# Optimization experiments

Hardware: AMD Instinct MI355X
Metric: run time of the kernel (lower is better)

Reference implementation:

```python
import jax, jax.numpy as jnp
import numpy as np
import math

N, E, IN, OUT, T, R = 50000, 500000, 128, 128, 8, 8
SQRT_DK = math.sqrt(OUT)


def setup_inputs() -> dict:
    key = jax.random.key(0)
    ks = jax.random.split(key, 12)
    return {
        "h": jax.random.normal(ks[0], (N, IN), jnp.float32),
        "adj": jax.random.randint(ks[1], (2, E), 0, N),
        "edge_type": jax.random.randint(ks[2], (E,), 0, R),
        "node_type": jax.random.randint(ks[3], (N,), 0, T),
        "src_type": jax.random.randint(ks[4], (E,), 0, T),
        "dst_type": jax.random.randint(ks[5], (E,), 0, T),
        # params (torch.rand -> uniform[0,1), torch.ones -> ones)
        "k_weights": jax.random.uniform(ks[6], (T, IN, OUT), jnp.float32),
        "q_weights": jax.random.uniform(ks[7], (T, IN, OUT), jnp.float32),
        "v_weights": jax.random.uniform(ks[8], (T, IN, OUT), jnp.float32),
        "a_weights": jax.random.uniform(ks[9], (T, OUT, OUT), jnp.float32),
        "relation_pri": jnp.ones((R, 1), jnp.float32),
        "relation_att": jax.random.uniform(ks[10], (R, OUT, OUT), jnp.float32),
        "relation_msg": jax.random.uniform(ks[11], (R, OUT, OUT), jnp.float32),
        "skip": jnp.ones((T,), jnp.float32),
    }


def _per_type(x, W, types):
    # x: [N,d], W: [T,d,f], types: [N] -> [N,f]
    # project by every type then select; avoids materializing a [N,d,f] gather
    all_proj = jnp.einsum('nd,tdf->tnf', x, W)  # [T,N,f]
    return all_proj[types, jnp.arange(x.shape[0])]


def _segment_softmax(scores, seg, num_segments):
    m = jax.ops.segment_max(scores, seg, num_segments=num_segments)
    m = jnp.where(jnp.isfinite(m), m, 0.0)  # empty segments
    ex = jnp.exp(scores - m[seg])
    denom = jax.ops.segment_sum(ex, seg, num_segments=num_segments)
    return ex / denom[seg]


def reference(h, adj, edge_type, node_type, src_type, dst_type,
              k_weights, q_weights, v_weights, a_weights,
              relation_pri, relation_att, relation_msg, skip):
    n = h.shape[0]
    src, dst = adj[0], adj[1]
    # per-node-type K/Q/V projections
    k = _per_type(h, k_weights, node_type)  # [N,OUT]
    q = _per_type(h, q_weights, node_type)
    v = _per_type(h, v_weights, node_type)
    # per-relation projections computed on nodes, then gathered per edge
    # (equivalent to k_j @ relation_att[edge_type] without an [E,D,D] gather)
    kA = jnp.einsum('nd,rdf->rnf', k, relation_att)[edge_type, src]  # [E,OUT]
    vM = jnp.einsum('nd,rdf->rnf', v, relation_msg)[edge_type, src]  # [E,OUT]
    q_i = q[dst]                                                     # [E,OUT]
    score = jnp.sum(kA * q_i, axis=-1) * relation_pri[edge_type, 0] / SQRT_DK  # [E]
    seg = dst * R + edge_type  # segment softmax keyed by (dst node, rel type)
    alpha = _segment_softmax(score, seg, n * R)  # [E]
    agg = jax.ops.segment_sum(vM * alpha[:, None], dst, num_segments=n)  # [N,OUT]
    # update: per-node-type output transform with sigmoid(skip) gate
    trans = _per_type(agg, a_weights, node_type)
    return trans * jax.nn.sigmoid(skip[node_type])[:, None]
```

## Files before the change

kernel.cpp:

```cpp
#include <hip/hip_runtime.h>
#include <math.h>


#define N_NODES 50000
#define N_EDGES 500000
#define DIM 128
#define TT 8
#define RR 8
#define RSQRT_DK 0.08838834764831845f

#define CHUNK_GRID 399
#define NODE_LIST_LEN (CHUNK_GRID * 128)
#define GRID_E ((N_EDGES + 255) / 256)
#define SCAN_BLOCKS ((N_NODES + 255) / 256)

#define NR3_CHUNKS 112
#define NR3_ROWS 448
#define NR3_ITERS 7

#define OFF_KA 0
#define OFF_HF 0
#define OFF_VM 25600000
#define OFF_KF 25600000
#define OFF_QF 51200000
#define OFF_AGGF 54400000
#define OFF_VF 54400000
#define OFF_ATTT 57600000
#define OFF_MSGT 57700000
#define OFF_WVT 57800000
#define OFF_WAT 57900000
#define OFF_INT 58000000
#define IO_NLIST 0
#define IO_CNT_N 51072
#define IO_CUR_N 51080
#define IO_POFF_N 51088
#define IO_DCNT 51104
#define IO_DCUR 101104
#define IO_DOFF 151104
#define IO_DPR 201104
#define IO_BLKSUM 701104
#define IO_BLKOFF 701360

typedef _Float16 half8 __attribute__((ext_vector_type(8)));
typedef _Float16 half4 __attribute__((ext_vector_type(4)));
typedef float f32x4 __attribute__((ext_vector_type(4)));

__global__ void init_kernel(int* wsi) {
    int i = blockIdx.x * blockDim.x + threadIdx.x;
    if (i < NODE_LIST_LEN) wsi[IO_NLIST + i] = -1;
    if (i < 32) wsi[IO_CNT_N + i] = 0;
    if (i < 100000) wsi[IO_DCNT + i] = 0;
}

__global__ void convert_kernel(const float* __restrict__ att,
                               const float* __restrict__ msg,
                               const float* __restrict__ Wv,
                               const float* __restrict__ Wa,
                               _Float16* __restrict__ attT,
                               _Float16* __restrict__ msgT,
                               _Float16* __restrict__ WvT,
                               _Float16* __restrict__ WaT) {
    int i = blockIdx.x * 256 + threadIdx.x;
    if (i >= RR * DIM * DIM) return;
    int td = i >> 14, d = (i >> 7) & 127, f = i & 127;
    int tr = (td << 14) + (f << 7) + d;
    attT[tr] = (_Float16)att[i];
    msgT[tr] = (_Float16)msg[i];
    WvT[tr] = (_Float16)Wv[i];
    WaT[tr] = (_Float16)Wa[i];
}

__global__ void hconv_kernel(const float* __restrict__ h,
                             _Float16* __restrict__ hF) {
    int i = blockIdx.x * 256 + threadIdx.x;
    if (i < N_NODES * DIM / 4) {
        float4 v = ((const float4*)h)[i];
        half4 o;
        o[0] = (_Float16)v.x; o[1] = (_Float16)v.y;
        o[2] = (_Float16)v.z; o[3] = (_Float16)v.w;
        *(half4*)(hF + (size_t)i * 4) = o;
    }
}

__global__ void hist_kernel(const int* __restrict__ ntype,
                            const int* __restrict__ adj, int* wsi) {
    __shared__ int cn[TT];
    int tid = threadIdx.x;
    if (tid < TT) cn[tid] = 0;
    __syncthreads();
    int i = blockIdx.x * blockDim.x + tid;
    if (i < N_NODES) atomicAdd(&cn[ntype[i]], 1);
    if (i < N_EDGES) atomicAdd(&wsi[IO_DCNT + adj[N_EDGES + i]], 1);
    __syncthreads();
    if (tid < TT && cn[tid] > 0) atomicAdd(&wsi[IO_CNT_N + tid], cn[tid]);
}

__global__ void offsets_kernel(int* wsi) {
    int off = 0;
    for (int t = 0; t < TT; ++t) {
        wsi[IO_POFF_N + t] = off;
        off += ((wsi[IO_CNT_N + t] + 127) >> 7) << 7;
    }
}

__global__ __launch_bounds__(256) void scanA_kernel(int* wsi) {
    __shared__ int tmp[256];
    int tid = threadIdx.x;
    int i = blockIdx.x * 256 + tid;
    int v = (i < N_NODES) ? wsi[IO_DCNT + i] : 0;
    tmp[tid] = v;
    __syncthreads();
    for (int off = 1; off < 256; off <<= 1) {
        int t = (tid >= off) ? tmp[tid - off] : 0;
        __syncthreads();
        tmp[tid] += t;
        __syncthreads();
    }
    if (i < N_NODES) wsi[IO_DOFF + i] = tmp[tid] - v;
    if (tid == 255) wsi[IO_BLKSUM + blockIdx.x] = tmp[255];
}

__global__ __launch_bounds__(256) void scanB_kernel(int* wsi) {
    __shared__ int tmp[256];
    int tid = threadIdx.x;
    int v = (tid < SCAN_BLOCKS) ? wsi[IO_BLKSUM + tid] : 0;
    tmp[tid] = v;
    __syncthreads();
    for (int off = 1; off < 256; off <<= 1) {
        int t = (tid >= off) ? tmp[tid - off] : 0;
        __syncthreads();
        tmp[tid] += t;
        __syncthreads();
    }
    wsi[IO_BLKOFF + tid] = tmp[tid] - v;
}

__global__ __launch_bounds__(256) void scanC_kernel(int* wsi) {
    int i = blockIdx.x * 256 + threadIdx.x;
    if (i < N_NODES) wsi[IO_DOFF + i] += wsi[IO_BLKOFF + blockIdx.x];
}

__global__ void scatter_kernel(const int* __restrict__ ntype,
                               const int* __restrict__ etype,
                               const int* __restrict__ adj, int* wsi) {
    __shared__ int cn[TT], bn[TT];
    int tid = threadIdx.x;
    if (tid < TT) cn[tid] = 0;
    __syncthreads();
    int i = blockIdx.x * blockDim.x + tid;
    int t = -1, rnk = 0;
    if (i < N_NODES) {
        t = ntype[i];
        rnk = atomicAdd(&cn[t], 1);
    }
    __syncthreads();
    if (tid < TT && cn[tid] > 0) bn[tid] = atomicAdd(&wsi[IO_CUR_N + tid], cn[tid]);
    __syncthreads();
    if (t >= 0)
        wsi[IO_NLIST + wsi[IO_POFF_N + t] + bn[t] + rnk] = i;
    if (i < N_EDGES) {
        int d = adj[N_EDGES + i];
        int pos = wsi[IO_DOFF + d] + atomicAdd(&wsi[IO_DCUR + d], 1);
        wsi[IO_DPR + pos] = (adj[i] << 3) | etype[i];
    }
}

__global__ __launch_bounds__(256, 4) void kq_f32_kernel(
    const float* __restrict__ h, const int* __restrict__ ntype,
    const float* __restrict__ Wk, const float* __restrict__ Wq,
    const int* __restrict__ nlist, _Float16* __restrict__ kout,
    _Float16* __restrict__ qout) {
    __shared__ float hl[64][DIM + 4];
    __shared__ int nid[64];
    int tid = threadIdx.x;
    int base = blockIdx.x * 64;
    if (tid < 64) nid[tid] = nlist[base + tid];
    __syncthreads();
    if (nid[0] < 0) return;
    int t = ntype[nid[0]];

    for (int r2 = 0; r2 < 64; r2 += 2) {
        int row = r2 + (tid >> 7);
        int col = tid & 127;
        int n = nid[row];
        if (n < 0) n = 0;
        hl[row][col] = h[(size_t)n * DIM + col];
    }
    __syncthreads();
    int te = tid >> 5, tc = tid & 31;

    int w = blockIdx.y;
    const float* W = (w == 0 ? Wk : Wq) + (size_t)t * DIM * DIM;
    const float4* W4 = (const float4*)W;
    _Float16* O = (w == 0 ? kout : qout);
    float acc[8][4] = {};
    float4 cur0 = W4[0 * 32 + tc];
    float4 cur1 = W4[1 * 32 + tc];
    float4 cur2 = W4[2 * 32 + tc];
    float4 cur3 = W4[3 * 32 + tc];
    for (int i = 0; i < DIM; i += 4) {
        int ip = (i + 4 < DIM) ? (i + 4) : 0;
        float4 nxt0 = W4[(ip + 0) * 32 + tc];
        float4 nxt1 = W4[(ip + 1) * 32 + tc];
        float4 nxt2 = W4[(ip + 2) * 32 + tc];
        float4 nxt3 = W4[(ip + 3) * 32 + tc];
#pragma unroll
        for (int j = 0; j < 8; ++j) {
            float4 hv = *(const float4*)&hl[te * 8 + j][i];
            acc[j][0] += hv.x * cur0.x;
            acc[j][1] += hv.x * cur0.y;
            acc[j][2] += hv.x * cur0.z;
            acc[j][3] += hv.x * cur0.w;
            acc[j][0] += hv.y * cur1.x;
            acc[j][1] += hv.y * cur1.y;
            acc[j][2] += hv.y * cur1.z;
            acc[j][3] += hv.y * cur1.w;
            acc[j][0] += hv.z * cur2.x;
            acc[j][1] += hv.z * cur2.y;
            acc[j][2] += hv.z * cur2.z;
            acc[j][3] += hv.z * cur2.w;
            acc[j][0] += hv.w * cur3.x;
            acc[j][1] += hv.w * cur3.y;
            acc[j][2] += hv.w * cur3.z;
            acc[j][3] += hv.w * cur3.w;
        }
        cur0 = nxt0;
        cur1 = nxt1;
        cur2 = nxt2;
        cur3 = nxt3;
    }
#pragma unroll
    for (int j = 0; j < 8; ++j) {
        int n = nid[te * 8 + j];
        if (n >= 0) {
            half4 o;
            o[0] = (_Float16)acc[j][0];
            o[1] = (_Float16)acc[j][1];
            o[2] = (_Float16)acc[j][2];
            o[3] = (_Float16)acc[j][3];
            *(half4*)(O + (size_t)n * DIM + tc * 4) = o;
        }
    }
}

__global__ __launch_bounds__(256) void vproj_kernel(
    const _Float16* __restrict__ hF, const int* __restrict__ ntype,
    const _Float16* __restrict__ WvT, const int* __restrict__ nlist,
    _Float16* __restrict__ vout) {
    __shared__ int nid[128];
    int tid = threadIdx.x;
    if (tid < 128) nid[tid] = nlist[blockIdx.x * 128 + tid];
    __syncthreads();
    if (nid[0] < 0) return;
    int t = ntype[nid[0]];
    int wv = tid >> 6, lane = tid & 63, l16 = lane & 15, quad = lane >> 4;
    int r0 = wv * 32;
    int nA[2];
#pragma unroll
    for (int m = 0; m < 2; ++m) nA[m] = nid[r0 + m * 16 + l16];
    const _Float16* B = WvT + (t << 14);
    f32x4 acc[2][8];
#pragma unroll
    for (int m = 0; m < 2; ++m)
#pragma unroll
        for (int c = 0; c < 8; ++c) acc[m][c] = (f32x4){0.f, 0.f, 0.f, 0.f};
    for (int kk = 0; kk < 4; ++kk) {
        int kb = kk * 32 + quad * 8;
        half8 a[2];
#pragma unroll
        for (int m = 0; m < 2; ++m)
            a[m] = (nA[m] >= 0)
                       ? *(const half8*)(hF + (size_t)nA[m] * DIM + kb)
                       : (half8){0, 0, 0, 0, 0, 0, 0, 0};
#pragma unroll
        for (int c = 0; c < 8; ++c) {
            half8 b = *(const half8*)(B + (c * 16 + l16) * DIM + kb);
#pragma unroll
            for (int m = 0; m < 2; ++m)
                acc[m][c] = __builtin_amdgcn_mfma_f32_16x16x32_f16(
                    a[m], b, acc[m][c], 0, 0, 0);
        }
    }
#pragma unroll
    for (int m = 0; m < 2; ++m)
#pragma unroll
        for (int c = 0; c < 8; ++c)
#pragma unroll
            for (int rg = 0; rg < 4; ++rg) {
                int node = nid[r0 + m * 16 + quad * 4 + rg];
                if (node >= 0)
                    vout[(size_t)node * DIM + c * 16 + l16] =
                        (_Float16)acc[m][c][rg];
            }
}

__global__ __launch_bounds__(256, 2) void nr_gemm3_kernel(
    const _Float16* __restrict__ A, const _Float16* __restrict__ B8,
    _Float16* __restrict__ Out, const float* __restrict__ pri, int isU) {
    __shared__ _Float16 stage[4][16][136];
    int bid = blockIdx.x;
    int rel = bid / NR3_CHUNKS;
    int chunk = bid - rel * NR3_CHUNKS;
    float scale = isU ? pri[rel] * RSQRT_DK : 1.0f;
    const _Float16* Bb = B8 + (rel << 14);
    int tid = threadIdx.x;
    int wv = tid >> 6, lane = tid & 63;
    int l16 = lane & 15, quad = lane >> 4;

    half8 bfrag[8][4];
#pragma unroll
    for (int c = 0; c < 8; ++c)
#pragma unroll
        for (int kk = 0; kk < 4; ++kk)
            bfrag[c][kk] =
                *(const half8*)(Bb + (c * 16 + l16) * DIM + kk * 32 + quad * 8);

    _Float16* Orel = Out + (size_t)rel * N_NODES * DIM;
    int base = chunk * NR3_ROWS + wv * 16;

    half8 aNow[4], aNext[4];
    {
        int nodeA = base + l16;
#pragma unroll
        for (int kk = 0; kk < 4; ++kk)
            aNow[kk] = (nodeA < N_NODES)
                           ? *(const half8*)(A + (size_t)nodeA * DIM +
                                             kk * 32 + quad * 8)
                           : (half8){0, 0, 0, 0, 0, 0, 0, 0};
    }

    for (int it = 0; it < NR3_ITERS; ++it) {
        int row0 = base + it * 64;
        if (it + 1 < NR3_ITERS) {
            int nodeA = row0 + 64 + l16;
#pragma unroll
            for (int kk = 0; kk < 4; ++kk)
                aNext[kk] = (nodeA < N_NODES)
                                ? *(const half8*)(A + (size_t)nodeA * DIM +
                                                  kk * 32 + quad * 8)
                                : (half8){0, 0, 0, 0, 0, 0, 0, 0};
        }
        f32x4 acc[8];
#pragma unroll
        for (int c = 0; c < 8; ++c) acc[c] = (f32x4){0.f, 0.f, 0.f, 0.f};
#pragma unroll
        for (int kk = 0; kk < 4; ++kk)
#pragma unroll
            for (int c = 0; c < 8; ++c)
                acc[c] = __builtin_amdgcn_mfma_f32_16x16x32_f16(
                    bfrag[c][kk], aNow[kk], acc[c], 0, 0, 0);
#pragma unroll
        for (int c = 0; c < 8; ++c) {
            half4 o;
#pragma unroll
            for (int rg = 0; rg < 4; ++rg)
                o[rg] = (_Float16)(acc[c][rg] * scale);
            *(half4*)&stage[wv][l16][c * 16 + quad * 4] = o;
        }
        _Float16* Op = Orel + (size_t)row0 * DIM;
#pragma unroll
        for (int s = 0; s < 4; ++s) {
            int row = s * 4 + quad;
            if (row0 + row < N_NODES) {
                half8 v = *(const half8*)&stage[wv][row][l16 * 8];
                *(half8*)(Op + (size_t)row * DIM + l16 * 8) = v;
            }
        }
#pragma unroll
        for (int kk = 0; kk < 4; ++kk) aNow[kk] = aNext[kk];
    }
}

__global__ __launch_bounds__(256) void attend_kernel(
    const _Float16* __restrict__ KA, const _Float16* __restrict__ qF,
    const _Float16* __restrict__ VMF, const int* __restrict__ dpr,
    const int* __restrict__ doff, const int* __restrict__ dcnt,
    _Float16* __restrict__ aggF) {
    int wv = threadIdx.x >> 6, lane = threadIdx.x & 63;
    int dst = blockIdx.x * 4 + wv;
    if (dst >= N_NODES) return;
    int l16 = lane & 15, g = lane >> 4, l8 = lane & 7;
    int beg = doff[dst], cnt = dcnt[dst];

    half8 qv = *(const half8*)(qF + (size_t)dst * DIM + l16 * 8);

    float m_own = -3e38f, sum_own = 0.f;
    float s0 = 0.f, s1 = 0.f, s2 = 0.f;
    int p0 = 0, p1 = 0, p2 = 0;

    for (int j0 = 0; j0 < cnt; j0 += 4) {
        int j = j0 + g;
        bool valid = j < cnt;
        int pr = valid ? dpr[beg + j] : 0;
        int src = pr >> 3, rel = pr & 7;
        half8 kv = *(const half8*)(KA + ((size_t)rel * N_NODES + src) * DIM +
                                   l16 * 8);
        float sa = 0.f, sb = 0.f;
#pragma unroll
        for (int i = 0; i < 4; ++i) sa += (float)kv[i] * (float)qv[i];
#pragma unroll
        for (int i = 4; i < 8; ++i) sb += (float)kv[i] * (float)qv[i];
        float s = sa + sb;
        s += __shfl_xor(s, 1, 16);
        s += __shfl_xor(s, 2, 16);
        s += __shfl_xor(s, 4, 16);
        s += __shfl_xor(s, 8, 16);
        if (!valid) s = -3e38f;
        int slot = j0 >> 6;
        int idx = (j0 >> 2) & 15;
        if (l16 == idx) {
            if (slot == 0) { s0 = s; p0 = pr; }
            else if (slot == 1) { s1 = s; p1 = pr; }
            else if (slot == 2) { s2 = s; p2 = pr; }
        }
        if (valid && l8 == rel) {
            if (s > m_own) {
                sum_own *= __expf(m_own - s);
                m_own = s;
            }
            sum_own += __expf(s - m_own);
        }
    }
    {
        float m2 = __shfl_xor(m_own, 16, 64);
        float t2 = __shfl_xor(sum_own, 16, 64);
        float mn = fmaxf(m_own, m2);
        sum_own = sum_own * __expf(m_own - mn) + t2 * __expf(m2 - mn);
        m_own = mn;
        m2 = __shfl_xor(m_own, 32, 64);
        t2 = __shfl_xor(sum_own, 32, 64);
        mn = fmaxf(m_own, m2);
        sum_own = sum_own * __expf(m_own - mn) + t2 * __expf(m2 - mn);
        m_own = mn;
    }
    float inv_own = (sum_own > 0.f) ? 1.f / sum_own : 0.f;

    float acc[8] = {0.f, 0.f, 0.f, 0.f, 0.f, 0.f, 0.f, 0.f};
    for (int j0 = 0; j0 < cnt; j0 += 4) {
        int j = j0 + g;
        bool valid = j < cnt;
        int slot = j0 >> 6;
        int idx = (j0 >> 2) & 15;
        float s;
        int pr;
        if (slot < 3) {
            float sv = (slot == 0) ? s0 : (slot == 1) ? s1 : s2;
            int pv = (slot == 0) ? p0 : (slot == 1) ? p1 : p2;
            s = __shfl(sv, idx, 16);
            pr = __shfl(pv, idx, 16);
        } else {
            pr = valid ? dpr[beg + j] : 0;
            int src = pr >> 3, rel = pr & 7;
            half8 kv = *(const half8*)(KA +
                                       ((size_t)rel * N_NODES + src) * DIM +
                                       l16 * 8);
            float sa = 0.f, sb = 0.f;
#pragma unroll
            for (int i = 0; i < 4; ++i) sa += (float)kv[i] * (float)qv[i];
#pragma unroll
            for (int i = 4; i < 8; ++i) sb += (float)kv[i] * (float)qv[i];
            s = sa + sb;
            s += __shfl_xor(s, 1, 16);
            s += __shfl_xor(s, 2, 16);
            s += __shfl_xor(s, 4, 16);
            s += __shfl_xor(s, 8, 16);
        }
        int rel = pr & 7, src = pr >> 3;
        float mr = __shfl(m_own, rel, 8);
        float iv = __shfl(inv_own, rel, 8);
        float alpha = valid ? __expf(s - mr) * iv : 0.f;
        half8 v = *(const half8*)(VMF + ((size_t)rel * N_NODES + src) * DIM +
                                  l16 * 8);
#pragma unroll
        for (int i = 0; i < 8; ++i) acc[i] += alpha * (float)v[i];
    }
#pragma unroll
    for (int i = 0; i < 8; ++i) {
        acc[i] += __shfl_xor(acc[i], 16, 64);
        acc[i] += __shfl_xor(acc[i], 32, 64);
    }
    if (g == 0) {
        half8 o;
#pragma unroll
        for (int i = 0; i < 8; ++i) o[i] = (_Float16)acc[i];
        *(half8*)(aggF + (size_t)dst * DIM + l16 * 8) = o;
    }
}

__global__ __launch_bounds__(256) void out_kernel(
    const _Float16* __restrict__ aggF, const int* __restrict__ ntype,
    const _Float16* __restrict__ WaT, const float* __restrict__ skip,
    const int* __restrict__ nlist, float* __restrict__ out) {
    __shared__ int nid[128];
    int tid = threadIdx.x;
    if (tid < 128) nid[tid] = nlist[blockIdx.x * 128 + tid];
    __syncthreads();
    if (nid[0] < 0) return;
    int t = ntype[nid[0]];
    float sig = 1.f / (1.f + __expf(-skip[t]));
    int wv = tid >> 6, lane = tid & 63, l16 = lane & 15, quad = lane >> 4;
    int r0 = wv * 32;
    int nA[2];
#pragma unroll
    for (int m = 0; m < 2; ++m) nA[m] = nid[r0 + m * 16 + l16];
    const _Float16* B = WaT + (t << 14);
    f32x4 acc[2][8];
#pragma unroll
    for (int m = 0; m < 2; ++m)
#pragma unroll
        for (int c = 0; c < 8; ++c) acc[m][c] = (f32x4){0.f, 0.f, 0.f, 0.f};
    for (int kk = 0; kk < 4; ++kk) {
        int kb = kk * 32 + quad * 8;
        half8 a[2];
#pragma unroll
        for (int m = 0; m < 2; ++m)
            a[m] = (nA[m] >= 0)
                       ? *(const half8*)(aggF + (size_t)nA[m] * DIM + kb)
                       : (half8){0, 0, 0, 0, 0, 0, 0, 0};
#pragma unroll
        for (int c = 0; c < 8; ++c) {
            half8 b = *(const half8*)(B + (c * 16 + l16) * DIM + kb);
#pragma unroll
            for (int m = 0; m < 2; ++m)
                acc[m][c] = __builtin_amdgcn_mfma_f32_16x16x32_f16(
                    a[m], b, acc[m][c], 0, 0, 0);
        }
    }
#pragma unroll
    for (int m = 0; m < 2; ++m)
#pragma unroll
        for (int c = 0; c < 8; ++c)
#pragma unroll
            for (int rg = 0; rg < 4; ++rg) {
                int node = nid[r0 + m * 16 + quad * 4 + rg];
                if (node >= 0)
                    out[(size_t)node * DIM + c * 16 + l16] =
                        acc[m][c][rg] * sig;
            }
}

extern "C" void kernel_launch(void* const* d_in, const int* in_sizes, int n_in,
                              void* d_out, int out_size, void* d_ws,
                              size_t ws_size, hipStream_t stream) {
    const float* h = (const float*)d_in[0];
    const int* adj = (const int*)d_in[1];
    const int* etype = (const int*)d_in[2];
    const int* ntype = (const int*)d_in[3];
    const float* Wk = (const float*)d_in[6];
    const float* Wq = (const float*)d_in[7];
    const float* Wv = (const float*)d_in[8];
    const float* Wa = (const float*)d_in[9];
    const float* pri = (const float*)d_in[10];
    const float* att = (const float*)d_in[11];
    const float* msg = (const float*)d_in[12];
    const float* skip = (const float*)d_in[13];
    float* out = (float*)d_out;

    int* wsi = (int*)d_ws + OFF_INT;
    _Float16* wsh = (_Float16*)d_ws;
    _Float16* KA = wsh + (size_t)OFF_KA * 2;
    _Float16* hF = wsh + (size_t)OFF_HF * 2;
    _Float16* VMF = wsh + (size_t)OFF_VM * 2;
    _Float16* kF = wsh + (size_t)OFF_KF * 2;
    _Float16* qF = wsh + (size_t)OFF_QF * 2;
    _Float16* aggF = wsh + (size_t)OFF_AGGF * 2;
    _Float16* vF = wsh + (size_t)OFF_VF * 2;
    _Float16* attT = wsh + (size_t)OFF_ATTT * 2;
    _Float16* msgT = wsh + (size_t)OFF_MSGT * 2;
    _Float16* WvT = wsh + (size_t)OFF_WVT * 2;
    _Float16* WaT = wsh + (size_t)OFF_WAT * 2;

    init_kernel<<<(100000 + 255) / 256, 256, 0, stream>>>(wsi);
    convert_kernel<<<(RR * DIM * DIM + 255) / 256, 256, 0, stream>>>(
        att, msg, Wv, Wa, attT, msgT, WvT, WaT);
    hconv_kernel<<<(N_NODES * DIM / 4 + 255) / 256, 256, 0, stream>>>(h, hF);
    hist_kernel<<<GRID_E, 256, 0, stream>>>(ntype, adj, wsi);
    offsets_kernel<<<1, 1, 0, stream>>>(wsi);
    scanA_kernel<<<SCAN_BLOCKS, 256, 0, stream>>>(wsi);
    scanB_kernel<<<1, 256, 0, stream>>>(wsi);
    scanC_kernel<<<SCAN_BLOCKS, 256, 0, stream>>>(wsi);
    scatter_kernel<<<GRID_E, 256, 0, stream>>>(ntype, etype, adj, wsi);
    {
        dim3 g(CHUNK_GRID * 2, 2);
        kq_f32_kernel<<<g, 256, 0, stream>>>(h, ntype, Wk, Wq,
                                             wsi + IO_NLIST, kF, qF);
    }
    vproj_kernel<<<CHUNK_GRID, 256, 0, stream>>>(hF, ntype, WvT,
                                                 wsi + IO_NLIST, vF);
    nr_gemm3_kernel<<<RR * NR3_CHUNKS, 256, 0, stream>>>(kF, attT, KA, pri, 1);
    nr_gemm3_kernel<<<RR * NR3_CHUNKS, 256, 0, stream>>>(vF, msgT, VMF, pri, 0);
    attend_kernel<<<(N_NODES + 3) / 4, 256, 0, stream>>>(
        KA, qF, VMF, wsi + IO_DPR, wsi + IO_DOFF, wsi + IO_DCNT, aggF);
    out_kernel<<<CHUNK_GRID, 256, 0, stream>>>(aggF, ntype, WaT, skip,
                                               wsi + IO_NLIST, out);
}
```

Measured before the change: 375.6 us.

## Compute K/Q projections with split-fp16 MFMA instead of FP32 FMA loops

Replaces the scalar FP32 K/Q projection kernel with an MFMA kernel that splits inputs and weights into fp16 hi/lo parts and sums three products (hi*hi, hi*lo, lo*hi) to keep near-FP32 accuracy. New conversion work writes the hLo residual for h and hi/lo transposed copies of Wk/Wq into the workspace. This trades extra memory traffic for the residual tensor, plus one extra launch, against moving the dominant FLOPs onto matrix cores. The output stores are scalar fp16 writes scattered per node row, which may be less efficient than the old vector stores.

```diff
diff --git a/kernel.cpp b/kernel.cpp
--- a/kernel.cpp
+++ b/kernel.cpp
@@ -22,6 +22,11 @@
 #define OFF_HF 0
 #define OFF_VM 25600000
 #define OFF_KF 25600000
+#define OFF_HLO 28800000
+#define OFF_WKHI 48000000
+#define OFF_WKLO 48100000
+#define OFF_WQHI 48200000
+#define OFF_WQLO 48300000
 #define OFF_QF 51200000
 #define OFF_AGGF 54400000
 #define OFF_VF 54400000
@@ -70,15 +75,41 @@
     WaT[tr] = (_Float16)Wa[i];
 }
 
+__global__ void convert2_kernel(const float* __restrict__ Wk,
+                                const float* __restrict__ Wq,
+                                _Float16* __restrict__ WkHiT,
+                                _Float16* __restrict__ WkLoT,
+                                _Float16* __restrict__ WqHiT,
+                                _Float16* __restrict__ WqLoT) {
+    int i = blockIdx.x * 256 + threadIdx.x;
+    if (i >= TT * DIM * DIM) return;
+    int td = i >> 14, d = (i >> 7) & 127, f = i & 127;
+    int tr = (td << 14) + (f << 7) + d;
+    float xk = Wk[i];
+    _Float16 hk = (_Float16)xk;
+    WkHiT[tr] = hk;
+    WkLoT[tr] = (_Float16)(xk - (float)hk);
+    float xq = Wq[i];
+    _Float16 hq = (_Float16)xq;
+    WqHiT[tr] = hq;
+    WqLoT[tr] = (_Float16)(xq - (float)hq);
+}
+
 __global__ void hconv_kernel(const float* __restrict__ h,
-                             _Float16* __restrict__ hF) {
+                             _Float16* __restrict__ hF,
+                             _Float16* __restrict__ hLo) {
     int i = blockIdx.x * 256 + threadIdx.x;
     if (i < N_NODES * DIM / 4) {
         float4 v = ((const float4*)h)[i];
-        half4 o;
+        half4 o, r;
         o[0] = (_Float16)v.x; o[1] = (_Float16)v.y;
         o[2] = (_Float16)v.z; o[3] = (_Float16)v.w;
+        r[0] = (_Float16)(v.x - (float)o[0]);
+        r[1] = (_Float16)(v.y - (float)o[1]);
+        r[2] = (_Float16)(v.z - (float)o[2]);
+        r[3] = (_Float16)(v.w - (float)o[3]);
         *(half4*)(hF + (size_t)i * 4) = o;
+        *(half4*)(hLo + (size_t)i * 4) = r;
     }
 }
 
@@ -165,82 +196,71 @@
     }
 }
 
-__global__ __launch_bounds__(256, 4) void kq_f32_kernel(
-    const float* __restrict__ h, const int* __restrict__ ntype,
-    const float* __restrict__ Wk, const float* __restrict__ Wq,
+__global__ __launch_bounds__(256) void kq_mfma_kernel(
+    const _Float16* __restrict__ hHi, const _Float16* __restrict__ hLo,
+    const int* __restrict__ ntype,
+    const _Float16* __restrict__ WkHiT, const _Float16* __restrict__ WkLoT,
+    const _Float16* __restrict__ WqHiT, const _Float16* __restrict__ WqLoT,
     const int* __restrict__ nlist, _Float16* __restrict__ kout,
     _Float16* __restrict__ qout) {
-    __shared__ float hl[64][DIM + 4];
-    __shared__ int nid[64];
-    int tid = threadIdx.x;
-    int base = blockIdx.x * 64;
-    if (tid < 64) nid[tid] = nlist[base + tid];
+    __shared__ int nid[128];
+    int tid = threadIdx.x;
+    if (tid < 128) nid[tid] = nlist[blockIdx.x * 128 + tid];
     __syncthreads();
     if (nid[0] < 0) return;
     int t = ntype[nid[0]];
-
-    for (int r2 = 0; r2 < 64; r2 += 2) {
-        int row = r2 + (tid >> 7);
-        int col = tid & 127;
-        int n = nid[row];
-        if (n < 0) n = 0;
-        hl[row][col] = h[(size_t)n * DIM + col];
-    }
-    __syncthreads();
-    int te = tid >> 5, tc = tid & 31;
-
+    int wv = tid >> 6, lane = tid & 63, l16 = lane & 15, quad = lane >> 4;
+    int r0 = wv * 32;
+    int nA[2];
+#pragma unroll
+    for (int m = 0; m < 2; ++m) nA[m] = nid[r0 + m * 16 + l16];
     int w = blockIdx.y;
-    const float* W = (w == 0 ? Wk : Wq) + (size_t)t * DIM * DIM;
-    const float4* W4 = (const float4*)W;
-    _Float16* O = (w == 0 ? kout : qout);
-    float acc[8][4] = {};
-    float4 cur0 = W4[0 * 32 + tc];
-    float4 cur1 = W4[1 * 32 + tc];
-    float4 cur2 = W4[2 * 32 + tc];
-    float4 cur3 = W4[3 * 32 + tc];
-    for (int i = 0; i < DIM; i += 4) {
-        int ip = (i + 4 < DIM) ? (i + 4) : 0;
-        float4 nxt0 = W4[(ip + 0) * 32 + tc];
-        float4 nxt1 = W4[(ip + 1) * 32 + tc];
-        float4 nxt2 = W4[(ip + 2) * 32 + tc];
-        float4 nxt3 = W4[(ip + 3) * 32 + tc];
-#pragma unroll
-        for (int j = 0; j < 8; ++j) {
-            float4 hv = *(const float4*)&hl[te * 8 + j][i];
-            acc[j][0] += hv.x * cur0.x;
-            acc[j][1] += hv.x * cur0.y;
-            acc[j][2] += hv.x * cur0.z;
-            acc[j][3] += hv.x * cur0.w;
-            acc[j][0] += hv.y * cur1.x;
-            acc[j][1] += hv.y * cur1.y;
-            acc[j][2] += hv.y * cur1.z;
-            acc[j][3] += hv.y * cur1.w;
-            acc[j][0] += hv.z * cur2.x;
-            acc[j][1] += hv.z * cur2.y;
-            acc[j][2] += hv.z * cur2.z;
-            acc[j][3] += hv.z * cur2.w;
-            acc[j][0] += hv.w * cur3.x;
-            acc[j][1] += hv.w * cur3.y;
-            acc[j][2] += hv.w * cur3.z;
-            acc[j][3] += hv.w * cur3.w;
-        }
-        cur0 = nxt0;
-        cur1 = nxt1;
-        cur2 = nxt2;
-        cur3 = nxt3;
-    }
-#pragma unroll
-    for (int j = 0; j < 8; ++j) {
-        int n = nid[te * 8 + j];
-        if (n >= 0) {
-            half4 o;
-            o[0] = (_Float16)acc[j][0];
-            o[1] = (_Float16)acc[j][1];
-            o[2] = (_Float16)acc[j][2];
-            o[3] = (_Float16)acc[j][3];
-            *(half4*)(O + (size_t)n * DIM + tc * 4) = o;
-        }
-    }
+    const _Float16* BHi = (w ? WqHiT : WkHiT) + (t << 14);
+    const _Float16* BLo = (w ? WqLoT : WkLoT) + (t << 14);
+    _Float16* O = w ? qout : kout;
+    f32x4 acc[2][8];
+#pragma unroll
+    for (int m = 0; m < 2; ++m)
+#pragma unroll
+        for (int c = 0; c < 8; ++c) acc[m][c] = (f32x4){0.f, 0.f, 0.f, 0.f};
+    for (int kk = 0; kk < 4; ++kk) {
+        int kb = kk * 32 + quad * 8;
+        half8 aHi[2], aLo[2];
+#pragma unroll
+        for (int m = 0; m < 2; ++m) {
+            aHi[m] = (nA[m] >= 0)
+                         ? *(const half8*)(hHi + (size_t)nA[m] * DIM + kb)
+                         : (half8){0, 0, 0, 0, 0, 0, 0, 0};
+            aLo[m] = (nA[m] >= 0)
+                         ? *(const half8*)(hLo + (size_t)nA[m] * DIM + kb)
+                         : (half8){0, 0, 0, 0, 0, 0, 0, 0};
+        }
+#pragma unroll
+        for (int c = 0; c < 8; ++c) {
+            half8 bHi = *(const half8*)(BHi + (c * 16 + l16) * DIM + kb);
+            half8 bLo = *(const half8*)(BLo + (c * 16 + l16) * DIM + kb);
+#pragma unroll
+            for (int m = 0; m < 2; ++m) {
+                acc[m][c] = __builtin_amdgcn_mfma_f32_16x16x32_f16(
+                    aHi[m], bHi, acc[m][c], 0, 0, 0);
+                acc[m][c] = __builtin_amdgcn_mfma_f32_16x16x32_f16(
+                    aHi[m], bLo, acc[m][c], 0, 0, 0);
+                acc[m][c] = __builtin_amdgcn_mfma_f32_16x16x32_f16(
+                    aLo[m], bHi, acc[m][c], 0, 0, 0);
+            }
+        }
+    }
+#pragma unroll
+    for (int m = 0; m < 2; ++m)
+#pragma unroll
+        for (int c = 0; c < 8; ++c)
+#pragma unroll
+            for (int rg = 0; rg < 4; ++rg) {
+                int node = nid[r0 + m * 16 + quad * 4 + rg];
+                if (node >= 0)
+                    O[(size_t)node * DIM + c * 16 + l16] =
+                        (_Float16)acc[m][c][rg];
+            }
 }
 
 __global__ __launch_bounds__(256) void vproj_kernel(
@@ -560,6 +580,7 @@
     _Float16* wsh = (_Float16*)d_ws;
     _Float16* KA = wsh + (size_t)OFF_KA * 2;
     _Float16* hF = wsh + (size_t)OFF_HF * 2;
+    _Float16* hLo = wsh + (size_t)OFF_HLO * 2;
     _Float16* VMF = wsh + (size_t)OFF_VM * 2;
     _Float16* kF = wsh + (size_t)OFF_KF * 2;
     _Float16* qF = wsh + (size_t)OFF_QF * 2;
@@ -569,11 +590,18 @@
     _Float16* msgT = wsh + (size_t)OFF_MSGT * 2;
     _Float16* WvT = wsh + (size_t)OFF_WVT * 2;
     _Float16* WaT = wsh + (size_t)OFF_WAT * 2;
+    _Float16* WkHiT = wsh + (size_t)OFF_WKHI * 2;
+    _Float16* WkLoT = wsh + (size_t)OFF_WKLO * 2;
+    _Float16* WqHiT = wsh + (size_t)OFF_WQHI * 2;
+    _Float16* WqLoT = wsh + (size_t)OFF_WQLO * 2;
 
     init_kernel<<<(100000 + 255) / 256, 256, 0, stream>>>(wsi);
     convert_kernel<<<(RR * DIM * DIM + 255) / 256, 256, 0, stream>>>(
         att, msg, Wv, Wa, attT, msgT, WvT, WaT);
-    hconv_kernel<<<(N_NODES * DIM / 4 + 255) / 256, 256, 0, stream>>>(h, hF);
+    convert2_kernel<<<(TT * DIM * DIM + 255) / 256, 256, 0, stream>>>(
+        Wk, Wq, WkHiT, WkLoT, WqHiT, WqLoT);
+    hconv_kernel<<<(N_NODES * DIM / 4 + 255) / 256, 256, 0, stream>>>(h, hF,
+                                                                      hLo);
     hist_kernel<<<GRID_E, 256, 0, stream>>>(ntype, adj, wsi);
     offsets_kernel<<<1, 1, 0, stream>>>(wsi);
     scanA_kernel<<<SCAN_BLOCKS, 256, 0, stream>>>(wsi);
@@ -581,9 +609,10 @@
     scanC_kernel<<<SCAN_BLOCKS, 256, 0, stream>>>(wsi);
     scatter_kernel<<<GRID_E, 256, 0, stream>>>(ntype, etype, adj, wsi);
     {
-        dim3 g(CHUNK_GRID * 2, 2);
-        kq_f32_kernel<<<g, 256, 0, stream>>>(h, ntype, Wk, Wq,
-                                             wsi + IO_NLIST, kF, qF);
+        dim3 g(CHUNK_GRID, 2);
+        kq_mfma_kernel<<<g, 256, 0, stream>>>(hF, hLo, ntype, WkHiT, WkLoT,
+                                              WqHiT, WqLoT, wsi + IO_NLIST,
+                                              kF, qF);
     }
     vproj_kernel<<<CHUNK_GRID, 256, 0, stream>>>(hF, ntype, WvT,
                                                  wsi + IO_NLIST, vF);
```

Result: slower. 383.2 us (+2.0%).
